# Kernel optimization log

Measured on AMD Instinct MI355X. Metric: run time of the kernel, lower is better.

Reference implementation:

```python
import jax, jax.numpy as jnp
import numpy as np

DIM = 256
HEADS = 4
HEAD_DIM = DIM // HEADS
SCALE = HEAD_DIM ** -0.5


def setup_inputs() -> dict:
    key = jax.random.key(0)
    ks = jax.random.split(key, 6)
    B, N, C = 4, 4096, DIM
    x = jax.random.normal(ks[0], (B, N, C), dtype=jnp.float32)
    # torch.nn.Linear weights are [out, in]; y = x @ W.T (+ b)
    s = 1.0 / np.sqrt(C)
    Wq = jax.random.uniform(ks[1], (C, C), jnp.float32, -s, s)
    Wk = jax.random.uniform(ks[2], (C, C), jnp.float32, -s, s)
    Wv = jax.random.uniform(ks[3], (C, C), jnp.float32, -s, s)
    Wp = jax.random.uniform(ks[4], (C, C), jnp.float32, -s, s)
    bp = jax.random.uniform(ks[5], (C,), jnp.float32, -s, s)
    return {"x": x, "Wq": Wq, "Wk": Wk, "Wv": Wv, "Wp": Wp, "bp": bp}


def reference(x, Wq, Wk, Wv, Wp, bp):
    B, N, C = x.shape
    H, D = HEADS, HEAD_DIM
    # project and split heads: [B, H, N, D]
    def heads(W):
        return (x @ W.T).reshape(B, N, H, D).transpose(0, 2, 1, 3)
    q = heads(Wq)
    k = heads(Wk)
    v = heads(Wv)
    attn = jnp.einsum('bhnd,bhmd->bhnm', q, k) * SCALE  # [B,H,N,N]
    attn = jax.nn.softmax(attn, axis=-1)
    out = jnp.einsum('bhnm,bhmd->bhnd', attn, v)  # [B,H,N,D]
    out = out.transpose(0, 2, 1, 3).reshape(B, N, C)
    return out @ Wp.T + bp
```

## Files before the change

### kernel.cpp

```cpp
#include <hip/hip_runtime.h>

typedef unsigned short u16t;
typedef unsigned int u32t;
typedef __bf16 bf16x8 __attribute__((ext_vector_type(8)));
typedef __bf16 bf16x4 __attribute__((ext_vector_type(4)));
typedef float f32x4 __attribute__((ext_vector_type(4)));
typedef unsigned int u32x4 __attribute__((ext_vector_type(4)));
typedef unsigned int u32x2 __attribute__((ext_vector_type(2)));

#define DEV static __device__ __forceinline__

DEV u16t f2bf(float f){
  u32t u = __builtin_bit_cast(u32t, f);
  u += 0x7fffu + ((u >> 16) & 1u);
  return (u16t)(u >> 16);
}

DEV u32t cvtpk(float lo, float hi){
  u32t r;
  asm("v_cvt_pk_bf16_f32 %0, %1, %2" : "=v"(r) : "v"(lo), "v"(hi));
  return r;
}

DEV float fexp2(float x){
#if __has_builtin(__builtin_amdgcn_exp2f)
  return __builtin_amdgcn_exp2f(x);
#else
  return exp2f(x);
#endif
}

DEV void gll16(const void* g, void* l){
  __builtin_amdgcn_global_load_lds((const __attribute__((address_space(1))) void*)g,
                                   (__attribute__((address_space(3))) void*)l, 16, 0, 0);
}

DEV f32x4 mfma16(bf16x8 a, bf16x8 b, f32x4 c){
  return __builtin_amdgcn_mfma_f32_16x16x32_bf16(a, b, c, 0, 0, 0);
}

DEV f32x4 mfma16k16(bf16x4 a, bf16x4 b, f32x4 c){
  asm("v_mfma_f32_16x16x16_bf16 %0, %1, %2, %0" : "+v"(c) : "v"(a), "v"(b));
  return c;
}

__global__ __launch_bounds__(256) void k_cast_x(const float4* __restrict__ x, u16t* __restrict__ xb){
  int idx = blockIdx.x * 256 + threadIdx.x;
  float4 v = x[idx];
  ushort4 o = make_ushort4(f2bf(v.x), f2bf(v.y), f2bf(v.z), f2bf(v.w));
  *(ushort4*)&xb[idx * 4] = o;
}

__global__ __launch_bounds__(256) void k_cast_w(const float* __restrict__ Wq, const float* __restrict__ Wk,
                         const float* __restrict__ Wv, const float* __restrict__ Wp,
                         u16t* __restrict__ wqkv, u16t* __restrict__ wp){
  int idx = blockIdx.x * 256 + threadIdx.x;
  if (idx < 196608){
    float v;
    if (idx < 65536)        v = Wq[idx] * 0.1803368801f;
    else if (idx < 131072)  v = Wk[idx - 65536];
    else                    v = Wv[idx - 131072];
    wqkv[idx] = f2bf(v);
  } else {
    int j = idx - 196608;
    wp[j] = f2bf(Wp[j]);
  }
}

template<bool IS_QKV>
__global__ __launch_bounds__(256) void k_gemm(const u16t* __restrict__ A, const u16t* __restrict__ W,
    const float* __restrict__ bias, u16t* __restrict__ oq, u16t* __restrict__ okk, u16t* __restrict__ ov,
    float* __restrict__ op, int Ntot){
  __shared__ u32x4 sm[1536];
  const int tid = threadIdx.x, lane = tid & 63, w = tid >> 6, g = lane >> 4, li = lane & 15;
  const int m0 = blockIdx.x * 128, n0 = blockIdx.y * 64;
  const int wm = w >> 1, wn = w & 1;
  f32x4 acc[4][2] = {};
  for (int kk = 0; kk < 4; ++kk){
    #pragma unroll
    for (int rnd = 0; rnd < 4; ++rnd){
      int cid = rnd * 256 + tid;
      int row = cid >> 3, ch = cid & 7;
      const u16t* src = A + (m0 + row) * 256 + kk * 64 + ((ch ^ (row & 7)) << 3);
      gll16(src, (char*)sm + (rnd * 256 + w * 64) * 16);
    }
    #pragma unroll
    for (int rnd = 0; rnd < 2; ++rnd){
      int cid = rnd * 256 + tid;
      int row = cid >> 3, ch = cid & 7;
      const u16t* src = W + (n0 + row) * 256 + kk * 64 + ((ch ^ (row & 7)) << 3);
      gll16(src, (char*)sm + 16384 + (rnd * 256 + w * 64) * 16);
    }
    __syncthreads();
    #pragma unroll
    for (int ks = 0; ks < 2; ++ks){
      bf16x8 bfr[2];
      #pragma unroll
      for (int nj = 0; nj < 2; ++nj){
        int row = wn * 32 + nj * 16 + li;
        bfr[nj] = __builtin_bit_cast(bf16x8, sm[1024 + row * 8 + ((ks * 4 + g) ^ (row & 7))]);
      }
      #pragma unroll
      for (int mi = 0; mi < 4; ++mi){
        int row = wm * 64 + mi * 16 + li;
        bf16x8 af = __builtin_bit_cast(bf16x8, sm[row * 8 + ((ks * 4 + g) ^ (row & 7))]);
        #pragma unroll
        for (int nj = 0; nj < 2; ++nj)
          acc[mi][nj] = mfma16(af, bfr[nj], acc[mi][nj]);
      }
    }
    __syncthreads();
  }
  if (IS_QKV){
    const int which = n0 >> 8, h = (n0 >> 6) & 3;
    if (which == 2){
      #pragma unroll
      for (int mi = 0; mi < 4; ++mi){
        int m = m0 + wm * 64 + mi * 16;
        int b = m >> 12, jt = (m & 4095) >> 4;
        int bh = b * 4 + h;
        #pragma unroll
        for (int nj = 0; nj < 2; ++nj){
          int dt = wn * 2 + nj;
          u32x2 pk;
          pk.x = cvtpk(acc[mi][nj][0], acc[mi][nj][1]);
          pk.y = cvtpk(acc[mi][nj][2], acc[mi][nj][3]);
          *(u32x2*)((char*)ov + (size_t)(((bh * 256 + jt) * 4 + dt) * 512) + lane * 8) = pk;
        }
      }
    } else {
      u16t* outp = which == 0 ? oq : okk;
      #pragma unroll
      for (int mi = 0; mi < 4; ++mi){
        int m = m0 + wm * 64 + mi * 16 + g * 4;
        int b = m >> 12, nn = m & 4095;
        #pragma unroll
        for (int nj = 0; nj < 2; ++nj){
          int d = wn * 32 + nj * 16 + li;
          #pragma unroll
          for (int r = 0; r < 4; ++r)
            outp[((b * 4 + h) * 4096 + nn + r) * 64 + d] = f2bf(acc[mi][nj][r]);
        }
      }
    }
  } else {
    #pragma unroll
    for (int mi = 0; mi < 4; ++mi){
      int m = m0 + wm * 64 + mi * 16 + g * 4;
      #pragma unroll
      for (int nj = 0; nj < 2; ++nj){
        int n = n0 + wn * 32 + nj * 16 + li;
        float bv = bias[n];
        #pragma unroll
        for (int r = 0; r < 4; ++r)
          op[(m + r) * Ntot + n] = acc[mi][nj][r] + bv;
      }
    }
  }
}

__global__ __launch_bounds__(256, 2) void k_flash(const u16t* __restrict__ q,
    const u16t* __restrict__ kg, const u16t* __restrict__ vp, u16t* __restrict__ ao){
  __shared__ u32x4 sm[2048];
  const int tid = threadIdx.x, lane = tid & 63, w = tid >> 6, g = lane >> 4, li = lane & 15;
  const int bid = blockIdx.x;
  const int swz = (bid & 7) * 64 + (bid >> 3);
  const int bh = swz >> 5, qt = swz & 31;
  const int rowbase = qt * 128 + w * 32;
  bf16x8 qf[2][2];
  #pragma unroll
  for (int f = 0; f < 2; ++f)
    #pragma unroll
    for (int ks = 0; ks < 2; ++ks)
      qf[f][ks] = __builtin_bit_cast(bf16x8,
        *(const u32x4*)&q[(bh * 4096 + rowbase + f * 16 + li) * 64 + ks * 32 + g * 8]);
  f32x4 ot[2][4] = {};
  f32x4 ls[2] = {};
  const u16t* kbase = kg + bh * 262144;
  const char* vbase = (const char*)vp + (size_t)bh * 524288;
  const bf16x4 vone = __builtin_bit_cast(bf16x4, (u32x2){0x3F803F80u, 0x3F803F80u});

  auto stage = [&](int t, int c){
    #pragma unroll
    for (int rnd = 0; rnd < 2; ++rnd){
      int cid = rnd * 256 + tid, row = cid >> 3, ch = cid & 7;
      gll16(kbase + (t * 64 + row) * 64 + ((ch ^ (row & 7)) << 3),
            (char*)sm + c * 8192 + cid * 16);
      gll16(vbase + t * 8192 + cid * 16,
            (char*)sm + 16384 + c * 8192 + cid * 16);
    }
  };

  stage(0, 0);
  __syncthreads();
  int cur = 0;
  #pragma unroll 1
  for (int t = 0; t < 64; ++t){
    if (t < 63) stage(t + 1, cur ^ 1);
    const u32x4* kb = sm + cur * 512;
    const char* vb = (const char*)sm + 16384 + cur * 8192;
    f32x4 st[2][4] = {};
    #pragma unroll
    for (int ks = 0; ks < 2; ++ks)
      #pragma unroll
      for (int jt = 0; jt < 4; ++jt){
        int row = jt * 16 + li;
        bf16x8 kf = __builtin_bit_cast(bf16x8, kb[row * 8 + ((ks * 4 + g) ^ (row & 7))]);
        st[0][jt] = mfma16(kf, qf[0][ks], st[0][jt]);
        st[1][jt] = mfma16(kf, qf[1][ks], st[1][jt]);
      }
    bf16x4 pa[2][4];
    #pragma unroll
    for (int f = 0; f < 2; ++f)
      #pragma unroll
      for (int jt = 0; jt < 4; ++jt){
        u32x2 pk;
        pk.x = cvtpk(fexp2(st[f][jt][0]), fexp2(st[f][jt][1]));
        pk.y = cvtpk(fexp2(st[f][jt][2]), fexp2(st[f][jt][3]));
        pa[f][jt] = __builtin_bit_cast(bf16x4, pk);
      }
    #pragma unroll
    for (int jt = 0; jt < 4; ++jt){
      #pragma unroll
      for (int dt = 0; dt < 4; ++dt){
        bf16x4 vf = *(const bf16x4*)(vb + (jt * 4 + dt) * 512 + lane * 8);
        ot[0][dt] = mfma16k16(pa[0][jt], vf, ot[0][dt]);
        ot[1][dt] = mfma16k16(pa[1][jt], vf, ot[1][dt]);
      }
      ls[0] = mfma16k16(pa[0][jt], vone, ls[0]);
      ls[1] = mfma16k16(pa[1][jt], vone, ls[1]);
    }
    __syncthreads();
    cur ^= 1;
  }
  const int b = bh >> 2, h = bh & 3;
  #pragma unroll
  for (int f = 0; f < 2; ++f){
    float inv[4];
    #pragma unroll
    for (int r = 0; r < 4; ++r)
      inv[r] = __builtin_amdgcn_rcpf(ls[f][r]);
    #pragma unroll
    for (int dt = 0; dt < 4; ++dt)
      #pragma unroll
      for (int r = 0; r < 4; ++r){
        int rowg = rowbase + f * 16 + 4 * g + r;
        ao[(b * 4096 + rowg) * 256 + h * 64 + dt * 16 + li] = f2bf(ot[f][dt][r] * inv[r]);
      }
  }
}

extern "C" void kernel_launch(void* const* d_in, const int* in_sizes, int n_in,
                              void* d_out, int out_size, void* d_ws, size_t ws_size,
                              hipStream_t stream){
  (void)in_sizes; (void)n_in; (void)out_size; (void)ws_size;
  const float* x  = (const float*)d_in[0];
  const float* Wq = (const float*)d_in[1];
  const float* Wk = (const float*)d_in[2];
  const float* Wv = (const float*)d_in[3];
  const float* Wp = (const float*)d_in[4];
  const float* bp = (const float*)d_in[5];
  float* out = (float*)d_out;

  u16t* ws   = (u16t*)d_ws;
  u16t* xb   = ws;
  u16t* qg   = ws + 4194304;
  u16t* kg   = ws + 8388608;
  u16t* vpk  = ws + 12582912;
  u16t* ao   = ws + 16777216;
  u16t* wqkv = ws + 20971520;
  u16t* wpb  = ws + 21168128;

  k_cast_x<<<4096, 256, 0, stream>>>((const float4*)x, xb);
  k_cast_w<<<1024, 256, 0, stream>>>(Wq, Wk, Wv, Wp, wqkv, wpb);
  k_gemm<true><<<dim3(128, 12), 256, 0, stream>>>(xb, wqkv, nullptr, qg, kg, vpk, nullptr, 768);
  k_flash<<<512, 256, 0, stream>>>(qg, kg, vpk, ao);
  k_gemm<false><<<dim3(128, 4), 256, 0, stream>>>(ao, wpb, bp, nullptr, nullptr, nullptr, out, 256);
}
```

Before: 116.2 us.

## Rewrite flash attention with 32x32 MFMA, transposed V, and triple-buffered staging

Switches the attention kernel from 16x16 MFMAs to 32x32x16 MFMAs, with each wave owning 64 query rows in a 128-thread block. V is now written transposed ([bh, d, n]) through LDS by the QKV GEMM epilogue. P is repacked in registers with v_permlane32_swap so it can feed the PV MFMA directly. The softmax denominator is now accumulated with VALU adds instead of extra ones-vector MFMAs, K/V staging moves to a three-buffer ring with explicit vmcnt waits, and the output goes out through an LDS-staged coalesced store. The aim is more MFMA throughput per instruction and fewer redundant MFMAs, at the cost of fewer waves per CU and higher register pressure.

```diff
diff --git a/kernel.cpp b/kernel.cpp
--- a/kernel.cpp
+++ b/kernel.cpp
@@ -3,8 +3,8 @@
 typedef unsigned short u16t;
 typedef unsigned int u32t;
 typedef __bf16 bf16x8 __attribute__((ext_vector_type(8)));
-typedef __bf16 bf16x4 __attribute__((ext_vector_type(4)));
 typedef float f32x4 __attribute__((ext_vector_type(4)));
+typedef float f32x16 __attribute__((ext_vector_type(16)));
 typedef unsigned int u32x4 __attribute__((ext_vector_type(4)));
 typedef unsigned int u32x2 __attribute__((ext_vector_type(2)));
 
@@ -20,6 +20,10 @@
   u32t r;
   asm("v_cvt_pk_bf16_f32 %0, %1, %2" : "=v"(r) : "v"(lo), "v"(hi));
   return r;
+}
+
+DEV void plswap(u32t &a, u32t &b){
+  asm("v_permlane32_swap_b32 %0, %1" : "+v"(a), "+v"(b));
 }
 
 DEV float fexp2(float x){
@@ -39,9 +43,8 @@
   return __builtin_amdgcn_mfma_f32_16x16x32_bf16(a, b, c, 0, 0, 0);
 }
 
-DEV f32x4 mfma16k16(bf16x4 a, bf16x4 b, f32x4 c){
-  asm("v_mfma_f32_16x16x16_bf16 %0, %1, %2, %0" : "+v"(c) : "v"(a), "v"(b));
-  return c;
+DEV f32x16 mfma32(bf16x8 a, bf16x8 b, f32x16 c){
+  return __builtin_amdgcn_mfma_f32_32x32x16_bf16(a, b, c, 0, 0, 0);
 }
 
 __global__ __launch_bounds__(256) void k_cast_x(const float4* __restrict__ x, u16t* __restrict__ xb){
@@ -69,7 +72,7 @@
 
 template<bool IS_QKV>
 __global__ __launch_bounds__(256) void k_gemm(const u16t* __restrict__ A, const u16t* __restrict__ W,
-    const float* __restrict__ bias, u16t* __restrict__ oq, u16t* __restrict__ okk, u16t* __restrict__ ov,
+    const float* __restrict__ bias, u16t* __restrict__ oq, u16t* __restrict__ okk, u16t* __restrict__ vtg,
     float* __restrict__ op, int Ntot){
   __shared__ u32x4 sm[1536];
   const int tid = threadIdx.x, lane = tid & 63, w = tid >> 6, g = lane >> 4, li = lane & 15;
@@ -114,19 +117,28 @@
   if (IS_QKV){
     const int which = n0 >> 8, h = (n0 >> 6) & 3;
     if (which == 2){
+      u16t* smv = (u16t*)sm;
       #pragma unroll
       for (int mi = 0; mi < 4; ++mi){
-        int m = m0 + wm * 64 + mi * 16;
-        int b = m >> 12, jt = (m & 4095) >> 4;
-        int bh = b * 4 + h;
         #pragma unroll
         for (int nj = 0; nj < 2; ++nj){
-          int dt = wn * 2 + nj;
-          u32x2 pk;
-          pk.x = cvtpk(acc[mi][nj][0], acc[mi][nj][1]);
-          pk.y = cvtpk(acc[mi][nj][2], acc[mi][nj][3]);
-          *(u32x2*)((char*)ov + (size_t)(((bh * 256 + jt) * 4 + dt) * 512) + lane * 8) = pk;
+          int d = wn * 32 + nj * 16 + li;
+          int mloc = wm * 64 + mi * 16 + g * 4;
+          u32x2 pk2;
+          pk2.x = cvtpk(acc[mi][nj][0], acc[mi][nj][1]);
+          pk2.y = cvtpk(acc[mi][nj][2], acc[mi][nj][3]);
+          int chk = mloc >> 3, inner = (mloc & 7) * 2;
+          *(u32x2*)((char*)smv + d * 256 + (((chk ^ (d & 7))) << 4) + inner) = pk2;
         }
+      }
+      __syncthreads();
+      const int b = m0 >> 12, bh2 = b * 4 + h, mbase = m0 & 4095;
+      #pragma unroll
+      for (int rnd = 0; rnd < 4; ++rnd){
+        int qq = rnd * 256 + tid;
+        int d = qq >> 4, ch = qq & 15;
+        *(u32x4*)&vtg[((size_t)bh2 * 64 + d) * 4096 + mbase + ch * 8] =
+            *(const u32x4*)((char*)smv + d * 256 + ((ch ^ (d & 7)) << 4));
       }
     } else {
       u16t* outp = which == 0 ? oq : okk;
@@ -159,94 +171,135 @@
   }
 }
 
-__global__ __launch_bounds__(256, 2) void k_flash(const u16t* __restrict__ q,
-    const u16t* __restrict__ kg, const u16t* __restrict__ vp, u16t* __restrict__ ao){
-  __shared__ u32x4 sm[2048];
-  const int tid = threadIdx.x, lane = tid & 63, w = tid >> 6, g = lane >> 4, li = lane & 15;
+__global__ __launch_bounds__(128, 1) void k_flash(const u16t* __restrict__ q,
+    const u16t* __restrict__ kg, const u16t* __restrict__ vtg, u16t* __restrict__ ao){
+  __shared__ char sm[49152];
+  const int tid = threadIdx.x, lane = tid & 63, w = tid >> 6;
+  const int hi = lane >> 5, p = lane & 31;
   const int bid = blockIdx.x;
   const int swz = (bid & 7) * 64 + (bid >> 3);
   const int bh = swz >> 5, qt = swz & 31;
-  const int rowbase = qt * 128 + w * 32;
-  bf16x8 qf[2][2];
+  const int rowbase = qt * 128 + w * 64;
+  const u16t* kb = kg + (size_t)bh * 262144;
+  const u16t* vb = vtg + (size_t)bh * 262144;
+
+  u32x4 qf[2][4];
   #pragma unroll
-  for (int f = 0; f < 2; ++f)
-    #pragma unroll
-    for (int ks = 0; ks < 2; ++ks)
-      qf[f][ks] = __builtin_bit_cast(bf16x8,
-        *(const u32x4*)&q[(bh * 4096 + rowbase + f * 16 + li) * 64 + ks * 32 + g * 8]);
-  f32x4 ot[2][4] = {};
-  f32x4 ls[2] = {};
-  const u16t* kbase = kg + bh * 262144;
-  const char* vbase = (const char*)vp + (size_t)bh * 524288;
-  const bf16x4 vone = __builtin_bit_cast(bf16x4, (u32x2){0x3F803F80u, 0x3F803F80u});
+  for (int it = 0; it < 2; ++it)
+    #pragma unroll
+    for (int kk = 0; kk < 4; ++kk)
+      qf[it][kk] = *(const u32x4*)&q[((size_t)bh * 4096 + rowbase + it * 32 + p) * 64 + kk * 16 + hi * 8];
+
+  f32x16 ot[2][2] = {};
+  float lsp[2][4] = {};
 
   auto stage = [&](int t, int c){
     #pragma unroll
-    for (int rnd = 0; rnd < 2; ++rnd){
-      int cid = rnd * 256 + tid, row = cid >> 3, ch = cid & 7;
-      gll16(kbase + (t * 64 + row) * 64 + ((ch ^ (row & 7)) << 3),
-            (char*)sm + c * 8192 + cid * 16);
-      gll16(vbase + t * 8192 + cid * 16,
-            (char*)sm + 16384 + c * 8192 + cid * 16);
+    for (int rnd = 0; rnd < 4; ++rnd){
+      int cid = rnd * 128 + tid;
+      int row = cid >> 3, ch = cid & 7;
+      gll16(kb + (t * 64 + row) * 64 + ((ch ^ (row & 7)) << 3), sm + c * 8192 + cid * 16);
+      gll16(vb + row * 4096 + t * 64 + ((ch ^ (row & 7)) << 3), sm + 24576 + c * 8192 + cid * 16);
     }
   };
 
+  auto compute = [&](int cbuf){
+    const char* kbuf = sm + cbuf * 8192;
+    const char* vbuf = sm + 24576 + cbuf * 8192;
+    f32x16 st[2][2] = {};
+    #pragma unroll
+    for (int kk = 0; kk < 4; ++kk)
+      #pragma unroll
+      for (int jt = 0; jt < 2; ++jt){
+        int row = jt * 32 + p;
+        bf16x8 kf = __builtin_bit_cast(bf16x8,
+            *(const u32x4*)(kbuf + row * 128 + (((kk * 2 + hi) ^ (row & 7)) << 4)));
+        st[0][jt] = mfma32(kf, __builtin_bit_cast(bf16x8, qf[0][kk]), st[0][jt]);
+        st[1][jt] = mfma32(kf, __builtin_bit_cast(bf16x8, qf[1][kk]), st[1][jt]);
+      }
+    u32x4 pf[2][2][2];
+    #pragma unroll
+    for (int it = 0; it < 2; ++it)
+      #pragma unroll
+      for (int jt = 0; jt < 2; ++jt){
+        float e[16];
+        #pragma unroll
+        for (int r = 0; r < 16; ++r)
+          e[r] = fexp2(st[it][jt][r]);
+        #pragma unroll
+        for (int r = 0; r < 16; ++r)
+          lsp[it][r & 3] += e[r];
+        #pragma unroll
+        for (int s = 0; s < 2; ++s){
+          u32t a0 = cvtpk(e[s*8+0], e[s*8+1]);
+          u32t a1 = cvtpk(e[s*8+2], e[s*8+3]);
+          u32t b0 = cvtpk(e[s*8+4], e[s*8+5]);
+          u32t b1 = cvtpk(e[s*8+6], e[s*8+7]);
+          plswap(a0, b0);
+          plswap(a1, b1);
+          pf[it][jt][s] = (u32x4){a0, a1, b0, b1};
+        }
+      }
+    #pragma unroll
+    for (int jt = 0; jt < 2; ++jt)
+      #pragma unroll
+      for (int s = 0; s < 2; ++s)
+        #pragma unroll
+        for (int dt = 0; dt < 2; ++dt){
+          int row = dt * 32 + p;
+          bf16x8 vf = __builtin_bit_cast(bf16x8,
+              *(const u32x4*)(vbuf + row * 128 + ((((jt * 2 + s) * 2 + hi) ^ (row & 7)) << 4)));
+          ot[0][dt] = mfma32(vf, __builtin_bit_cast(bf16x8, pf[0][jt][s]), ot[0][dt]);
+          ot[1][dt] = mfma32(vf, __builtin_bit_cast(bf16x8, pf[1][jt][s]), ot[1][dt]);
+        }
+  };
+
   stage(0, 0);
+  stage(1, 1);
+  int c = 0;
+  #pragma unroll 1
+  for (int t = 0; t < 63; ++t){
+    asm volatile("s_waitcnt vmcnt(8)" ::: "memory");
+    __builtin_amdgcn_s_barrier();
+    asm volatile("" ::: "memory");
+    int nb = c + 2; if (nb > 2) nb -= 3;
+    if (t < 62) stage(t + 2, nb);
+    compute(c);
+    c = (c == 2) ? 0 : c + 1;
+  }
+  asm volatile("s_waitcnt vmcnt(0)" ::: "memory");
+  __builtin_amdgcn_s_barrier();
+  asm volatile("" ::: "memory");
+  compute(c);
   __syncthreads();
-  int cur = 0;
-  #pragma unroll 1
-  for (int t = 0; t < 64; ++t){
-    if (t < 63) stage(t + 1, cur ^ 1);
-    const u32x4* kb = sm + cur * 512;
-    const char* vb = (const char*)sm + 16384 + cur * 8192;
-    f32x4 st[2][4] = {};
-    #pragma unroll
-    for (int ks = 0; ks < 2; ++ks)
-      #pragma unroll
-      for (int jt = 0; jt < 4; ++jt){
-        int row = jt * 16 + li;
-        bf16x8 kf = __builtin_bit_cast(bf16x8, kb[row * 8 + ((ks * 4 + g) ^ (row & 7))]);
-        st[0][jt] = mfma16(kf, qf[0][ks], st[0][jt]);
-        st[1][jt] = mfma16(kf, qf[1][ks], st[1][jt]);
-      }
-    bf16x4 pa[2][4];
-    #pragma unroll
-    for (int f = 0; f < 2; ++f)
-      #pragma unroll
-      for (int jt = 0; jt < 4; ++jt){
-        u32x2 pk;
-        pk.x = cvtpk(fexp2(st[f][jt][0]), fexp2(st[f][jt][1]));
-        pk.y = cvtpk(fexp2(st[f][jt][2]), fexp2(st[f][jt][3]));
-        pa[f][jt] = __builtin_bit_cast(bf16x4, pk);
-      }
-    #pragma unroll
-    for (int jt = 0; jt < 4; ++jt){
-      #pragma unroll
-      for (int dt = 0; dt < 4; ++dt){
-        bf16x4 vf = *(const bf16x4*)(vb + (jt * 4 + dt) * 512 + lane * 8);
-        ot[0][dt] = mfma16k16(pa[0][jt], vf, ot[0][dt]);
-        ot[1][dt] = mfma16k16(pa[1][jt], vf, ot[1][dt]);
-      }
-      ls[0] = mfma16k16(pa[0][jt], vone, ls[0]);
-      ls[1] = mfma16k16(pa[1][jt], vone, ls[1]);
-    }
-    __syncthreads();
-    cur ^= 1;
-  }
+
+  float inv[2];
+  #pragma unroll
+  for (int it = 0; it < 2; ++it){
+    float l4 = (lsp[it][0] + lsp[it][1]) + (lsp[it][2] + lsp[it][3]);
+    l4 += __shfl_xor(l4, 32);
+    inv[it] = __builtin_amdgcn_rcpf(l4);
+  }
+  char* smw = sm + w * 8192;
+  #pragma unroll
+  for (int it = 0; it < 2; ++it)
+    #pragma unroll
+    for (int dt = 0; dt < 2; ++dt)
+      #pragma unroll
+      for (int k2 = 0; k2 < 8; ++k2){
+        int d0 = ((2*k2) & 3) + 8 * ((2*k2) >> 2) + 4 * hi + dt * 32;
+        u32t pk = cvtpk(ot[it][dt][2*k2] * inv[it], ot[it][dt][2*k2+1] * inv[it]);
+        int row = it * 32 + p;
+        int colb = d0 * 2;
+        *(u32t*)(smw + row * 128 + (((colb >> 4) ^ (row & 7)) << 4) + (colb & 15)) = pk;
+      }
   const int b = bh >> 2, h = bh & 3;
   #pragma unroll
-  for (int f = 0; f < 2; ++f){
-    float inv[4];
-    #pragma unroll
-    for (int r = 0; r < 4; ++r)
-      inv[r] = __builtin_amdgcn_rcpf(ls[f][r]);
-    #pragma unroll
-    for (int dt = 0; dt < 4; ++dt)
-      #pragma unroll
-      for (int r = 0; r < 4; ++r){
-        int rowg = rowbase + f * 16 + 4 * g + r;
-        ao[(b * 4096 + rowg) * 256 + h * 64 + dt * 16 + li] = f2bf(ot[f][dt][r] * inv[r]);
-      }
+  for (int rnd = 0; rnd < 8; ++rnd){
+    int qq = rnd * 64 + lane;
+    int row = qq >> 3, ch = qq & 7;
+    u32x4 v = *(const u32x4*)(smw + row * 128 + ((ch ^ (row & 7)) << 4));
+    *(u32x4*)&ao[((size_t)b * 4096 + rowbase + row) * 256 + h * 64 + ch * 8] = v;
   }
 }
 
@@ -266,14 +319,14 @@
   u16t* xb   = ws;
   u16t* qg   = ws + 4194304;
   u16t* kg   = ws + 8388608;
-  u16t* vpk  = ws + 12582912;
+  u16t* vtg  = ws + 12582912;
   u16t* ao   = ws + 16777216;
   u16t* wqkv = ws + 20971520;
   u16t* wpb  = ws + 21168128;
 
   k_cast_x<<<4096, 256, 0, stream>>>((const float4*)x, xb);
   k_cast_w<<<1024, 256, 0, stream>>>(Wq, Wk, Wv, Wp, wqkv, wpb);
-  k_gemm<true><<<dim3(128, 12), 256, 0, stream>>>(xb, wqkv, nullptr, qg, kg, vpk, nullptr, 768);
-  k_flash<<<512, 256, 0, stream>>>(qg, kg, vpk, ao);
+  k_gemm<true><<<dim3(128, 12), 256, 0, stream>>>(xb, wqkv, nullptr, qg, kg, vtg, nullptr, 768);
+  k_flash<<<512, 128, 0, stream>>>(qg, kg, vtg, ao);
   k_gemm<false><<<dim3(128, 4), 256, 0, stream>>>(ao, wpb, bp, nullptr, nullptr, nullptr, out, 256);
 }
```

Result: faster. 113.9 us (-2.0%).
